# Kernel tuning notes

Measured on AMD Instinct MI355X. Metric: run time of the kernel, lower is better.

Reference implementation:

```python
import jax, jax.numpy as jnp
import numpy as np

D_LOW = 32
LAGS = [1, 2, 4, 8]
# Upper-triangular pair indices (offset=1), matching torch.triu_indices(d_low, d_low, 1)
IDX_I, IDX_J = np.triu_indices(D_LOW, k=1)
IDX_I = jnp.asarray(IDX_I)
IDX_J = jnp.asarray(IDX_J)
EPS = 1e-6


def setup_inputs() -> dict:
    key = jax.random.key(0)
    ks = jax.random.split(key, 7)
    b, n, d_model = 4, 4096, 1024
    d_plucker = D_LOW * (D_LOW - 1) // 2  # 496
    s = lambda fan_in: 1.0 / np.sqrt(fan_in)
    return {
        "x": jax.random.normal(ks[0], (b, n, d_model), dtype=jnp.float32),
        "W_red": jax.random.normal(ks[1], (d_model, D_LOW), dtype=jnp.float32) * s(d_model),
        "b_red": jax.random.normal(ks[2], (D_LOW,), dtype=jnp.float32) * s(d_model),
        "W_exp": jax.random.normal(ks[3], (d_plucker, d_model), dtype=jnp.float32) * s(d_plucker),
        "b_exp": jax.random.normal(ks[4], (d_model,), dtype=jnp.float32) * s(d_plucker),
        "W_gate": jax.random.normal(ks[5], (2 * d_model, d_model), dtype=jnp.float32) * s(2 * d_model),
        "b_gate": jax.random.normal(ks[6], (d_model,), dtype=jnp.float32) * s(2 * d_model),
    }


def reference(x, W_red, b_red, W_exp, b_exp, W_gate, b_gate):
    b, n, _ = x.shape
    d_plucker = D_LOW * (D_LOW - 1) // 2
    z = x @ W_red + b_red  # [b, n, d_low]
    plucker_total = jnp.zeros((b, n, d_plucker), dtype=x.dtype)
    counts = jnp.zeros((b, n, 1), dtype=x.dtype)
    for lag in LAGS:
        if lag <= 0 or lag >= n:
            continue
        z_curr = z[:, lag:, :]   # [b, n-lag, d_low]
        z_past = z[:, :-lag, :]  # [b, n-lag, d_low]
        # Antisymmetric Plucker coordinates over upper-triangular index pairs
        p = (z_curr[:, :, IDX_I] * z_past[:, :, IDX_J]
             - z_curr[:, :, IDX_J] * z_past[:, :, IDX_I])  # [b, n-lag, d_plucker]
        norm = jnp.linalg.norm(p, axis=-1, keepdims=True)
        p = p / jnp.maximum(norm, EPS)
        plucker_total = plucker_total.at[:, lag:, :].add(p)
        counts = counts.at[:, lag:, :].add(1.0)
    counts = jnp.maximum(counts, 1.0)
    plucker_avg = plucker_total / counts
    g_avg = plucker_avg @ W_exp + b_exp  # [b, n, d_model]
    concat = jnp.concatenate([x, g_avg], axis=-1)  # [b, n, 2*d_model]
    gate = jax.nn.sigmoid(concat @ W_gate + b_gate)
    return gate * x + (1.0 - gate) * g_avg
```

## Files before the change

### kernel.cpp

```cpp
#include <hip/hip_runtime.h>
#include <hip/hip_bf16.h>
#include <math.h>

#define B_DIM   4
#define N_DIM   4096
#define D_MODEL 1024
#define D_LOW   32
#define NPAIR   496
#define NROWS   (B_DIM * N_DIM)
#define KPAD3   512
#define LDA2    1536

typedef __bf16 bf16;
typedef __bf16 bf16x8 __attribute__((ext_vector_type(8)));
typedef __bf16 bf16x4 __attribute__((ext_vector_type(4)));
typedef float  f32x4  __attribute__((ext_vector_type(4)));

#define GLOAD_LDS16(g, l) __builtin_amdgcn_global_load_lds( \
    (__attribute__((address_space(1))) void*)(g),           \
    (__attribute__((address_space(3))) void*)(l), 16, 0, 0)

__global__ __launch_bounds__(256) void wred_t(const float* __restrict__ Wr,
                                              bf16* __restrict__ WrT) {
    __shared__ float tile[32][33];
    const int t  = threadIdx.x;
    const int kb = blockIdx.x * 32;
    {
        int k = t >> 3, c4 = (t & 7) * 4;
        float4 v = *reinterpret_cast<const float4*>(&Wr[(size_t)(kb + k) * 32 + c4]);
        tile[k][c4 + 0] = v.x; tile[k][c4 + 1] = v.y;
        tile[k][c4 + 2] = v.z; tile[k][c4 + 3] = v.w;
    }
    __syncthreads();
    {
        int c = t >> 3, kq = (t & 7) * 4;
        bf16x4 o = { (bf16)tile[kq + 0][c], (bf16)tile[kq + 1][c],
                     (bf16)tile[kq + 2][c], (bf16)tile[kq + 3][c] };
        *reinterpret_cast<bf16x4*>(&WrT[(size_t)c * 1024 + kb + kq]) = o;
    }
}

__global__ __launch_bounds__(256) void k1_mfma(const float* __restrict__ x,
                                               const bf16* __restrict__ WrT,
                                               bf16* __restrict__ a2,
                                               float* __restrict__ zpart) {
    const int t    = threadIdx.x;
    const int wv   = t >> 6, lane = t & 63;
    const int l15  = lane & 15, lhi = lane >> 4;
    const int kc   = blockIdx.x;
    const int mt   = blockIdx.y;
    const int row  = mt * 64 + wv * 16 + l15;
    const int kb   = kc * 512;

    f32x4 accz[2] = { (f32x4){0.f,0.f,0.f,0.f}, (f32x4){0.f,0.f,0.f,0.f} };

#pragma unroll
    for (int ks = 0; ks < 16; ++ks) {
        const int k0 = kb + ks * 32 + lhi * 8;
        const float4 u0 = *reinterpret_cast<const float4*>(&x[(size_t)row * 1024 + k0]);
        const float4 u1 = *reinterpret_cast<const float4*>(&x[(size_t)row * 1024 + k0 + 4]);
        bf16x8 af = { (bf16)u0.x, (bf16)u0.y, (bf16)u0.z, (bf16)u0.w,
                      (bf16)u1.x, (bf16)u1.y, (bf16)u1.z, (bf16)u1.w };
        *reinterpret_cast<bf16x8*>(&a2[(size_t)row * LDA2 + k0]) = af;
        const bf16x8 b0 = *reinterpret_cast<const bf16x8*>(
            &WrT[(size_t)l15 * 1024 + kb + ks * 32 + lhi * 8]);
        const bf16x8 b1 = *reinterpret_cast<const bf16x8*>(
            &WrT[(size_t)(16 + l15) * 1024 + kb + ks * 32 + lhi * 8]);
        accz[0] = __builtin_amdgcn_mfma_f32_16x16x32_bf16(af, b0, accz[0], 0, 0, 0);
        accz[1] = __builtin_amdgcn_mfma_f32_16x16x32_bf16(af, b1, accz[1], 0, 0, 0);
    }
#pragma unroll
    for (int cg = 0; cg < 2; ++cg)
#pragma unroll
        for (int r = 0; r < 4; ++r) {
            const int rout = mt * 64 + wv * 16 + lhi * 4 + r;
            zpart[((size_t)kc * NROWS + rout) * 32 + cg * 16 + l15] = accz[cg][r];
        }
}

__global__ __launch_bounds__(256) void k2_plucker(const float* __restrict__ zpart,
                                                  const float* __restrict__ br,
                                                  bf16* __restrict__ a2) {
    const int wv   = threadIdx.x >> 6;
    const int lane = threadIdx.x & 63;
    const int row  = blockIdx.x * 4 + wv;
    const int t    = row & (N_DIM - 1);
    const int c    = lane & 31;
    const float bias = br[c];

    float zc = bias;
#pragma unroll
    for (int p = 0; p < 2; ++p)
        zc += zpart[((size_t)p * NROWS + row) * 32 + c];

    float zp[4];
    float red[9];
    red[0] = zc * zc;
#pragma unroll
    for (int li = 0; li < 4; ++li) {
        const int lag = 1 << li;
        float v = 0.f;
        if (t >= lag) {
            v = bias;
#pragma unroll
            for (int p = 0; p < 2; ++p)
                v += zpart[((size_t)p * NROWS + (row - lag)) * 32 + c];
        }
        zp[li] = v;
        red[1 + li] = zc * zp[li];
        red[5 + li] = zp[li] * zp[li];
    }
#pragma unroll
    for (int m = 1; m < 32; m <<= 1) {
#pragma unroll
        for (int i = 0; i < 9; ++i) red[i] += __shfl_xor(red[i], m);
    }
    float cnt = 0.f;
#pragma unroll
    for (int li = 0; li < 4; ++li) cnt += (t >= (1 << li)) ? 1.f : 0.f;
    const float inv = 1.f / fmaxf(cnt, 1.f);

    float w = 0.f;
#pragma unroll
    for (int li = 0; li < 4; ++li) {
        float n2 = fmaxf(red[0] * red[5 + li] - red[1 + li] * red[1 + li], 0.f);
        float nr = sqrtf(n2);
        float s  = (t >= (1 << li)) ? inv / fmaxf(nr, 1e-6f) : 0.f;
        w += s * zp[li];
    }

#pragma unroll
    for (int u = 0; u < 8; ++u) {
        const int k = u * 64 + lane;
        float v = 0.f;
        if (k < NPAIR) {
            int kk = k, i = 0;
            while (kk >= 31 - i) { kk -= 31 - i; ++i; }
            const int j = i + 1 + kk;
            float zci = __shfl(zc, i), zcj = __shfl(zc, j);
            float wi  = __shfl(w, i),  wj  = __shfl(w, j);
            v = zci * wj - zcj * wi;
        }
        a2[(size_t)row * LDA2 + 1024 + k] = (bf16)v;
    }
}

__global__ __launch_bounds__(256) void transpose_cvt(const float* __restrict__ src,
                                                     bf16* __restrict__ dst,
                                                     int Ksrc, int Kpad) {
    __shared__ float tile[32][36];
    const int t  = threadIdx.x;
    const int kb = blockIdx.x * 32;
    const int nb = blockIdx.y * 32;
    int li = t * 4;
    int kl = li >> 5, nl = li & 31;
    float4 v = {0.f, 0.f, 0.f, 0.f};
    if (kb + kl < Ksrc)
        v = *reinterpret_cast<const float4*>(&src[(size_t)(kb + kl) * 1024 + nb + nl]);
    tile[kl][nl + 0] = v.x; tile[kl][nl + 1] = v.y;
    tile[kl][nl + 2] = v.z; tile[kl][nl + 3] = v.w;
    __syncthreads();
    int nl2 = li >> 5, kl2 = li & 31;
    bf16x4 o = { (bf16)tile[kl2 + 0][nl2], (bf16)tile[kl2 + 1][nl2],
                 (bf16)tile[kl2 + 2][nl2], (bf16)tile[kl2 + 3][nl2] };
    *reinterpret_cast<bf16x4*>(&dst[(size_t)(nb + nl2) * Kpad + kb + kl2]) = o;
}

__global__ __launch_bounds__(256) void we_cvt_be(const float* __restrict__ We,
                                                 const float* __restrict__ be,
                                                 bf16* __restrict__ WeB) {
    size_t o = ((size_t)blockIdx.x * 256 + threadIdx.x) * 4;
    int row = (int)(o >> 10), col = (int)(o & 1023);
    float4 v = {0.f, 0.f, 0.f, 0.f};
    if (row < NPAIR)      v = *reinterpret_cast<const float4*>(&We[(size_t)row * 1024 + col]);
    else if (row == NPAIR) v = *reinterpret_cast<const float4*>(&be[col]);
    bf16x4 b = { (bf16)v.x, (bf16)v.y, (bf16)v.z, (bf16)v.w };
    *reinterpret_cast<bf16x4*>(&WeB[o]) = b;
}

__global__ __launch_bounds__(256) void wcomb_mfma(const bf16* __restrict__ A,
                                                  const bf16* __restrict__ Bt,
                                                  bf16* __restrict__ BcT) {
    __shared__ bf16 As[128 * 32];
    __shared__ bf16 Bs[128 * 32];
    const int t    = threadIdx.x;
    const int mb   = blockIdx.y * 128;
    const int nbq  = blockIdx.x * 128;
    const int w    = t >> 6, lane = t & 63;
    const int wr   = w >> 1, wc = w & 1;
    const int l15  = lane & 15, lhi = lane >> 4;

    f32x4 acc[4][4];
#pragma unroll
    for (int mt = 0; mt < 4; ++mt)
#pragma unroll
        for (int nt = 0; nt < 4; ++nt) acc[mt][nt] = (f32x4){0.f, 0.f, 0.f, 0.f};

    const int li0 = t, li1 = t + 256;
    const int r0 = li0 >> 2, c0 = (li0 & 3) * 8;
    const int r1 = li1 >> 2, c1 = (li1 & 3) * 8;

    for (int kb = 0; kb < 1024; kb += 32) {
        GLOAD_LDS16(A  + (size_t)(mb + r0) * 1024 + kb + c0, As + li0 * 8);
        GLOAD_LDS16(A  + (size_t)(mb + r1) * 1024 + kb + c1, As + li1 * 8);
        GLOAD_LDS16(Bt + (size_t)(nbq + r0) * 1024 + kb + c0, Bs + li0 * 8);
        GLOAD_LDS16(Bt + (size_t)(nbq + r1) * 1024 + kb + c1, Bs + li1 * 8);
        __syncthreads();
        bf16x8 a[4], b[4];
#pragma unroll
        for (int mt = 0; mt < 4; ++mt)
            a[mt] = *reinterpret_cast<const bf16x8*>(
                As + (wr * 64 + mt * 16 + l15) * 32 + lhi * 8);
#pragma unroll
        for (int nt = 0; nt < 4; ++nt)
            b[nt] = *reinterpret_cast<const bf16x8*>(
                Bs + (wc * 64 + nt * 16 + l15) * 32 + lhi * 8);
#pragma unroll
        for (int mt = 0; mt < 4; ++mt)
#pragma unroll
            for (int nt = 0; nt < 4; ++nt)
                acc[mt][nt] = __builtin_amdgcn_mfma_f32_16x16x32_bf16(
                    a[mt], b[nt], acc[mt][nt], 0, 0, 0);
        __syncthreads();
    }
#pragma unroll
    for (int mt = 0; mt < 4; ++mt)
#pragma unroll
        for (int nt = 0; nt < 4; ++nt) {
            const int col = nbq + wc * 64 + nt * 16 + l15;
#pragma unroll
            for (int r = 0; r < 4; ++r) {
                const int row = mb + wr * 64 + mt * 16 + lhi * 4 + r;
                BcT[(size_t)row * 1536 + 1024 + col] = (bf16)acc[mt][nt][r];
            }
        }
}

__global__ __launch_bounds__(256) void bgc_extract(const float* __restrict__ bg,
                                                   const bf16* __restrict__ BcT,
                                                   float* __restrict__ bgc) {
    int n = blockIdx.x * 256 + threadIdx.x;
    bgc[n] = bg[n] + (float)BcT[(size_t)n * 1536 + 1024 + NPAIR];
}

template <int KDIM, int LDAp, int LDBp, bool GATE>
__global__ __launch_bounds__(512, 2) void gemmzr(const bf16* __restrict__ A,
                                                 const bf16* __restrict__ Bt,
                                                 const float* __restrict__ bias,
                                                 const bf16* __restrict__ gsrc,
                                                 bf16* __restrict__ gdst,
                                                 float* __restrict__ out) {
    extern __shared__ char lds[];
    const int t    = threadIdx.x;
    const int w    = t >> 6, lane = t & 63;
    const int wr   = w >> 2, wc = w & 3;
    const int l15  = lane & 15, lhi = lane >> 4;

    const int fid = blockIdx.x;
    const int xcd = fid & 7, loc = fid >> 3;
    const int mb  = (xcd * 8 + (loc >> 2)) * 256;
    const int nb  = (loc & 3) * 256;

    const int srow = t >> 3;
    const int scol = ((t & 7) ^ (srow & 7)) * 8;
    const size_t aOff = (size_t)(mb + srow) * LDAp + scol;
    const size_t bOff = (size_t)(nb + srow) * LDBp + scol;
    char* const ldsA = lds;
    char* const ldsB = lds + 65536;

#define STAGE_A(d, h, kb) do { \
    GLOAD_LDS16(A + aOff + (size_t)((h) * 128) * LDAp + (kb),      ldsA + (d) * 32768 + (h) * 16384 + t * 16); \
    GLOAD_LDS16(A + aOff + (size_t)((h) * 128 + 64) * LDAp + (kb), ldsA + (d) * 32768 + (h) * 16384 + 8192 + t * 16); } while (0)
#define STAGE_B(d, h, kb) do { \
    GLOAD_LDS16(Bt + bOff + (size_t)((h) * 128) * LDBp + (kb),      ldsB + (d) * 32768 + (h) * 16384 + t * 16); \
    GLOAD_LDS16(Bt + bOff + (size_t)((h) * 128 + 64) * LDBp + (kb), ldsB + (d) * 32768 + (h) * 16384 + 8192 + t * 16); } while (0)

    const int swx = (l15 & 7) << 4;
#define LDAF(d, mq_) do { const char* Ab_ = ldsA + (d) * 32768 + wr * 16384; \
    _Pragma("unroll") for (int mf = 0; mf < 4; ++mf) \
    _Pragma("unroll") for (int ks = 0; ks < 2; ++ks) { \
        int lin = ((mq_) * 64 + mf * 16 + l15) * 128 + ks * 64 + lhi * 16; \
        afr[mf][ks] = *reinterpret_cast<const bf16x8*>(Ab_ + (lin ^ swx)); } } while (0)
#define LDBF(dst, d, nq_) do { const char* Bb_ = ldsB + (d) * 32768 + (wc >> 1) * 16384; \
    _Pragma("unroll") for (int nf = 0; nf < 2; ++nf) \
    _Pragma("unroll") for (int ks = 0; ks < 2; ++ks) { \
        int lin = ((wc & 1) * 64 + (nq_) * 32 + nf * 16 + l15) * 128 + ks * 64 + lhi * 16; \
        dst[nf][ks] = *reinterpret_cast<const bf16x8*>(Bb_ + (lin ^ swx)); } } while (0)
#define MMA(bset, mq_, nq_) do { __builtin_amdgcn_s_setprio(1); \
    _Pragma("unroll") for (int mf = 0; mf < 4; ++mf) \
    _Pragma("unroll") for (int nf = 0; nf < 2; ++nf) \
    _Pragma("unroll") for (int ks = 0; ks < 2; ++ks) \
        acc[(mq_) * 4 + mf][(nq_) * 2 + nf] = __builtin_amdgcn_mfma_f32_16x16x32_bf16( \
            afr[mf][ks], bset[nf][ks], acc[(mq_) * 4 + mf][(nq_) * 2 + nf], 0, 0, 0); \
    __builtin_amdgcn_s_setprio(0); } while (0)
#define BAR() asm volatile("s_barrier" ::: "memory")

    f32x4 acc[8][4];
#pragma unroll
    for (int i = 0; i < 8; ++i)
#pragma unroll
        for (int j = 0; j < 4; ++j) acc[i][j] = (f32x4){0.f, 0.f, 0.f, 0.f};
    bf16x8 afr[4][2], bfr0[2][2], bfrB[2][2];

    STAGE_A(0, 0, 0);  STAGE_A(0, 1, 0);  STAGE_B(0, 0, 0);  STAGE_B(0, 1, 0);
    STAGE_A(1, 0, 64); STAGE_A(1, 1, 64); STAGE_B(1, 0, 64); STAGE_B(1, 1, 64);

    const int NT    = KDIM / 64;
    const int ITERS = NT / 2;
    for (int it = 0; it < ITERS; ++it) {
        const int kA = (it * 2 + 2) * 64;
        const int kB = (it * 2 + 3) * 64;
        const bool p2 = (it * 2 + 2) < NT;
        const bool p3 = (it * 2 + 3) < NT;

        asm volatile("s_waitcnt vmcnt(8)" ::: "memory");
        BAR();
        LDAF(0, 0); LDBF(bfr0, 0, 0);
        MMA(bfr0, 0, 0);
        BAR();
        LDBF(bfrB, 0, 1);
        MMA(bfrB, 0, 1);
        BAR();
        if (p2) { STAGE_B(0, 0, kA); STAGE_B(0, 1, kA); }
        LDAF(0, 1);
        MMA(bfrB, 1, 1);
        BAR();
        if (p2) { STAGE_A(0, 0, kA); STAGE_A(0, 1, kA); }
        MMA(bfr0, 1, 0);

        if (p2) asm volatile("s_waitcnt vmcnt(8)" ::: "memory");
        else    asm volatile("s_waitcnt vmcnt(0)" ::: "memory");
        BAR();
        LDAF(1, 0); LDBF(bfr0, 1, 0);
        MMA(bfr0, 0, 0);
        BAR();
        LDBF(bfrB, 1, 1);
        MMA(bfrB, 0, 1);
        BAR();
        if (p3) { STAGE_B(1, 0, kB); STAGE_B(1, 1, kB); }
        LDAF(1, 1);
        MMA(bfrB, 1, 1);
        BAR();
        if (p3) { STAGE_A(1, 0, kB); STAGE_A(1, 1, kB); }
        MMA(bfr0, 1, 0);
    }
#undef STAGE_A
#undef STAGE_B
#undef LDAF
#undef LDBF
#undef MMA
#undef BAR

#pragma unroll
    for (int mi = 0; mi < 8; ++mi) {
#pragma unroll
        for (int nf = 0; nf < 4; ++nf) {
            const int col = nb + wc * 64 + nf * 16 + l15;
            const float bv = bias[col];
#pragma unroll
            for (int r = 0; r < 4; ++r) {
                const int row = mb + wr * 128 + mi * 16 + lhi * 4 + r;
                float v = acc[mi][nf][r] + bv;
                if constexpr (GATE) {
                    float gate = 1.f / (1.f + expf(-v));
                    float xv = (float)A[(size_t)row * LDAp + col];
                    float gv = (float)gsrc[(size_t)row * D_MODEL + col];
                    out[(size_t)row * D_MODEL + col] = gate * xv + (1.f - gate) * gv;
                } else {
                    gdst[(size_t)row * D_MODEL + col] = (bf16)v;
                }
            }
        }
    }
}

extern "C" void kernel_launch(void* const* d_in, const int* in_sizes, int n_in,
                              void* d_out, int out_size, void* d_ws, size_t ws_size,
                              hipStream_t stream) {
    const float* x  = (const float*)d_in[0];
    const float* Wr = (const float*)d_in[1];
    const float* br = (const float*)d_in[2];
    const float* We = (const float*)d_in[3];
    const float* be = (const float*)d_in[4];
    const float* Wg = (const float*)d_in[5];
    const float* bg = (const float*)d_in[6];
    float* out = (float*)d_out;

    char* ws = (char*)d_ws;
    bf16*  gbuf  = (bf16*)(ws);
    float* zpart = (float*)(ws);
    bf16*  A2    = (bf16*)(ws + (32u << 20));
    bf16*  WeT   = (bf16*)(ws + (80u << 20));
    bf16*  BcT   = (bf16*)(ws + (81u << 20));
    bf16*  WgbT  = (bf16*)(ws + (84u << 20));
    bf16*  WeB   = (bf16*)(ws + (86u << 20));
    float* bgc   = (float*)(ws + (87u << 20));
    bf16*  WrT   = (bf16*)(ws + (88u << 20));

    (void)hipFuncSetAttribute(reinterpret_cast<const void*>(&gemmzr<KPAD3, LDA2, KPAD3, false>),
                              hipFuncAttributeMaxDynamicSharedMemorySize, 131072);
    (void)hipFuncSetAttribute(reinterpret_cast<const void*>(&gemmzr<1536, LDA2, 1536, true>),
                              hipFuncAttributeMaxDynamicSharedMemorySize, 131072);

    wred_t<<<32, 256, 0, stream>>>(Wr, WrT);
    k1_mfma<<<dim3(2, 256), 256, 0, stream>>>(x, WrT, A2, zpart);
    k2_plucker<<<NROWS / 4, 256, 0, stream>>>(zpart, br, A2);

    transpose_cvt<<<dim3(KPAD3 / 32, 1024 / 32), 256, 0, stream>>>(We, WeT, NPAIR, KPAD3);
    transpose_cvt<<<dim3(1024 / 32, 1024 / 32), 256, 0, stream>>>(Wg, BcT, 1024, 1536);
    transpose_cvt<<<dim3(1024 / 32, 1024 / 32), 256, 0, stream>>>(Wg + (size_t)1024 * 1024, WgbT, 1024, 1024);
    we_cvt_be<<<512, 256, 0, stream>>>(We, be, WeB);
    wcomb_mfma<<<dim3(4, 8), 256, 0, stream>>>(WgbT, WeB, BcT);
    bgc_extract<<<4, 256, 0, stream>>>(bg, BcT, bgc);

    gemmzr<KPAD3, LDA2, KPAD3, false><<<256, 512, 131072, stream>>>(
        A2 + 1024, WeT, be, nullptr, gbuf, nullptr);
    gemmzr<1536, LDA2, 1536, true><<<256, 512, 131072, stream>>>(
        A2, BcT, bgc, gbuf, nullptr, out);
}
```

Before: 164.6 us.

## Merge weight-prep kernels and fold gate bias extraction into GEMM epilogue

Cuts the launch count of the weight-preparation stage. The Wr transpose and the We/be conversion become one kernel, and the three transpose_cvt calls become one 3D-grid kernel. The weight-combine GEMM is rewritten as a smaller per-wave MFMA kernel with no LDS and many more blocks, and the separate bias-extract kernel is dropped by reading the folded bias column inside the gated GEMM epilogue. The aim is lower launch and serialization overhead plus better parallelism for the small GEMM, at the cost of uncached direct global loads in the combine kernel.

```diff
diff --git a/kernel.cpp b/kernel.cpp
--- a/kernel.cpp
+++ b/kernel.cpp
@@ -20,23 +20,37 @@
     (__attribute__((address_space(1))) void*)(g),           \
     (__attribute__((address_space(3))) void*)(l), 16, 0, 0)
 
-__global__ __launch_bounds__(256) void wred_t(const float* __restrict__ Wr,
-                                              bf16* __restrict__ WrT) {
+__global__ __launch_bounds__(256) void prep_misc(const float* __restrict__ Wr,
+                                                 bf16* __restrict__ WrT,
+                                                 const float* __restrict__ We,
+                                                 const float* __restrict__ be,
+                                                 bf16* __restrict__ WeB) {
     __shared__ float tile[32][33];
+    const int bx = blockIdx.x;
     const int t  = threadIdx.x;
-    const int kb = blockIdx.x * 32;
-    {
-        int k = t >> 3, c4 = (t & 7) * 4;
-        float4 v = *reinterpret_cast<const float4*>(&Wr[(size_t)(kb + k) * 32 + c4]);
-        tile[k][c4 + 0] = v.x; tile[k][c4 + 1] = v.y;
-        tile[k][c4 + 2] = v.z; tile[k][c4 + 3] = v.w;
-    }
-    __syncthreads();
-    {
-        int c = t >> 3, kq = (t & 7) * 4;
-        bf16x4 o = { (bf16)tile[kq + 0][c], (bf16)tile[kq + 1][c],
-                     (bf16)tile[kq + 2][c], (bf16)tile[kq + 3][c] };
-        *reinterpret_cast<bf16x4*>(&WrT[(size_t)c * 1024 + kb + kq]) = o;
+    if (bx < 32) {
+        const int kb = bx * 32;
+        {
+            int k = t >> 3, c4 = (t & 7) * 4;
+            float4 v = *reinterpret_cast<const float4*>(&Wr[(size_t)(kb + k) * 32 + c4]);
+            tile[k][c4 + 0] = v.x; tile[k][c4 + 1] = v.y;
+            tile[k][c4 + 2] = v.z; tile[k][c4 + 3] = v.w;
+        }
+        __syncthreads();
+        {
+            int c = t >> 3, kq = (t & 7) * 4;
+            bf16x4 o = { (bf16)tile[kq + 0][c], (bf16)tile[kq + 1][c],
+                         (bf16)tile[kq + 2][c], (bf16)tile[kq + 3][c] };
+            *reinterpret_cast<bf16x4*>(&WrT[(size_t)c * 1024 + kb + kq]) = o;
+        }
+    } else {
+        size_t o = ((size_t)(bx - 32) * 256 + t) * 4;
+        int row = (int)(o >> 10), col = (int)(o & 1023);
+        float4 v = {0.f, 0.f, 0.f, 0.f};
+        if (row < NPAIR)       v = *reinterpret_cast<const float4*>(&We[(size_t)row * 1024 + col]);
+        else if (row == NPAIR) v = *reinterpret_cast<const float4*>(&be[col]);
+        bf16x4 b = { (bf16)v.x, (bf16)v.y, (bf16)v.z, (bf16)v.w };
+        *reinterpret_cast<bf16x4*>(&WeB[o]) = b;
     }
 }
 
@@ -145,13 +159,21 @@
     }
 }
 
-__global__ __launch_bounds__(256) void transpose_cvt(const float* __restrict__ src,
-                                                     bf16* __restrict__ dst,
-                                                     int Ksrc, int Kpad) {
+__global__ __launch_bounds__(256) void transpose2(const float* __restrict__ Wg,
+                                                  const float* __restrict__ We,
+                                                  bf16* __restrict__ BcT,
+                                                  bf16* __restrict__ WgbT,
+                                                  bf16* __restrict__ WeT) {
     __shared__ float tile[32][36];
+    const int z = blockIdx.z;
+    const float* src = (z == 0) ? Wg : (z == 1) ? (Wg + (size_t)1024 * 1024) : We;
+    bf16* dst  = (z == 0) ? BcT : (z == 1) ? WgbT : WeT;
+    const int Kpad = (z == 0) ? 1536 : (z == 1) ? 1024 : 512;
+    const int Ksrc = (z == 2) ? NPAIR : 1024;
+    const int kb = blockIdx.x * 32;
+    if (kb >= Kpad) return;
+    const int nb = blockIdx.y * 32;
     const int t  = threadIdx.x;
-    const int kb = blockIdx.x * 32;
-    const int nb = blockIdx.y * 32;
     int li = t * 4;
     int kl = li >> 5, nl = li & 31;
     float4 v = {0.f, 0.f, 0.f, 0.f};
@@ -166,81 +188,28 @@
     *reinterpret_cast<bf16x4*>(&dst[(size_t)(nb + nl2) * Kpad + kb + kl2]) = o;
 }
 
-__global__ __launch_bounds__(256) void we_cvt_be(const float* __restrict__ We,
-                                                 const float* __restrict__ be,
-                                                 bf16* __restrict__ WeB) {
-    size_t o = ((size_t)blockIdx.x * 256 + threadIdx.x) * 4;
-    int row = (int)(o >> 10), col = (int)(o & 1023);
-    float4 v = {0.f, 0.f, 0.f, 0.f};
-    if (row < NPAIR)      v = *reinterpret_cast<const float4*>(&We[(size_t)row * 1024 + col]);
-    else if (row == NPAIR) v = *reinterpret_cast<const float4*>(&be[col]);
-    bf16x4 b = { (bf16)v.x, (bf16)v.y, (bf16)v.z, (bf16)v.w };
-    *reinterpret_cast<bf16x4*>(&WeB[o]) = b;
-}
-
-__global__ __launch_bounds__(256) void wcomb_mfma(const bf16* __restrict__ A,
-                                                  const bf16* __restrict__ Bt,
+__global__ __launch_bounds__(256) void wcomb_wave(const bf16* __restrict__ WgbT,
+                                                  const bf16* __restrict__ WeB,
                                                   bf16* __restrict__ BcT) {
-    __shared__ bf16 As[128 * 32];
-    __shared__ bf16 Bs[128 * 32];
     const int t    = threadIdx.x;
-    const int mb   = blockIdx.y * 128;
-    const int nbq  = blockIdx.x * 128;
-    const int w    = t >> 6, lane = t & 63;
-    const int wr   = w >> 1, wc = w & 1;
+    const int wv   = t >> 6, lane = t & 63;
     const int l15  = lane & 15, lhi = lane >> 4;
-
-    f32x4 acc[4][4];
-#pragma unroll
-    for (int mt = 0; mt < 4; ++mt)
-#pragma unroll
-        for (int nt = 0; nt < 4; ++nt) acc[mt][nt] = (f32x4){0.f, 0.f, 0.f, 0.f};
-
-    const int li0 = t, li1 = t + 256;
-    const int r0 = li0 >> 2, c0 = (li0 & 3) * 8;
-    const int r1 = li1 >> 2, c1 = (li1 & 3) * 8;
-
+    const int kk0  = blockIdx.x * 16;
+    const int n0   = blockIdx.y * 64 + wv * 16;
+    f32x4 acc = (f32x4){0.f, 0.f, 0.f, 0.f};
+#pragma unroll 8
     for (int kb = 0; kb < 1024; kb += 32) {
-        GLOAD_LDS16(A  + (size_t)(mb + r0) * 1024 + kb + c0, As + li0 * 8);
-        GLOAD_LDS16(A  + (size_t)(mb + r1) * 1024 + kb + c1, As + li1 * 8);
-        GLOAD_LDS16(Bt + (size_t)(nbq + r0) * 1024 + kb + c0, Bs + li0 * 8);
-        GLOAD_LDS16(Bt + (size_t)(nbq + r1) * 1024 + kb + c1, Bs + li1 * 8);
-        __syncthreads();
-        bf16x8 a[4], b[4];
-#pragma unroll
-        for (int mt = 0; mt < 4; ++mt)
-            a[mt] = *reinterpret_cast<const bf16x8*>(
-                As + (wr * 64 + mt * 16 + l15) * 32 + lhi * 8);
-#pragma unroll
-        for (int nt = 0; nt < 4; ++nt)
-            b[nt] = *reinterpret_cast<const bf16x8*>(
-                Bs + (wc * 64 + nt * 16 + l15) * 32 + lhi * 8);
-#pragma unroll
-        for (int mt = 0; mt < 4; ++mt)
-#pragma unroll
-            for (int nt = 0; nt < 4; ++nt)
-                acc[mt][nt] = __builtin_amdgcn_mfma_f32_16x16x32_bf16(
-                    a[mt], b[nt], acc[mt][nt], 0, 0, 0);
-        __syncthreads();
-    }
-#pragma unroll
-    for (int mt = 0; mt < 4; ++mt)
-#pragma unroll
-        for (int nt = 0; nt < 4; ++nt) {
-            const int col = nbq + wc * 64 + nt * 16 + l15;
-#pragma unroll
-            for (int r = 0; r < 4; ++r) {
-                const int row = mb + wr * 64 + mt * 16 + lhi * 4 + r;
-                BcT[(size_t)row * 1536 + 1024 + col] = (bf16)acc[mt][nt][r];
-            }
-        }
-}
-
-__global__ __launch_bounds__(256) void bgc_extract(const float* __restrict__ bg,
-                                                   const bf16* __restrict__ BcT,
-                                                   float* __restrict__ bgc) {
-    int n = blockIdx.x * 256 + threadIdx.x;
-    bgc[n] = bg[n] + (float)BcT[(size_t)n * 1536 + 1024 + NPAIR];
+        const bf16x8 af = *reinterpret_cast<const bf16x8*>(
+            &WgbT[(size_t)(n0 + l15) * 1024 + kb + lhi * 8]);
+        const bf16x8 bf = *reinterpret_cast<const bf16x8*>(
+            &WeB[(size_t)(kk0 + l15) * 1024 + kb + lhi * 8]);
+        acc = __builtin_amdgcn_mfma_f32_16x16x32_bf16(af, bf, acc, 0, 0, 0);
+    }
+#pragma unroll
+    for (int r = 0; r < 4; ++r) {
+        const int n = n0 + lhi * 4 + r;
+        BcT[(size_t)n * 1536 + 1024 + kk0 + l15] = (bf16)acc[r];
+    }
 }
 
 template <int KDIM, int LDAp, int LDBp, bool GATE>
@@ -356,7 +325,9 @@
 #pragma unroll
         for (int nf = 0; nf < 4; ++nf) {
             const int col = nb + wc * 64 + nf * 16 + l15;
-            const float bv = bias[col];
+            float bv = bias[col];
+            if constexpr (GATE)
+                bv += (float)Bt[(size_t)col * LDBp + 1024 + NPAIR];
 #pragma unroll
             for (int r = 0; r < 4; ++r) {
                 const int row = mb + wr * 128 + mi * 16 + lhi * 4 + r;
@@ -394,7 +365,6 @@
     bf16*  BcT   = (bf16*)(ws + (81u << 20));
     bf16*  WgbT  = (bf16*)(ws + (84u << 20));
     bf16*  WeB   = (bf16*)(ws + (86u << 20));
-    float* bgc   = (float*)(ws + (87u << 20));
     bf16*  WrT   = (bf16*)(ws + (88u << 20));
 
     (void)hipFuncSetAttribute(reinterpret_cast<const void*>(&gemmzr<KPAD3, LDA2, KPAD3, false>),
@@ -402,19 +372,14 @@
     (void)hipFuncSetAttribute(reinterpret_cast<const void*>(&gemmzr<1536, LDA2, 1536, true>),
                               hipFuncAttributeMaxDynamicSharedMemorySize, 131072);
 
-    wred_t<<<32, 256, 0, stream>>>(Wr, WrT);
+    prep_misc<<<544, 256, 0, stream>>>(Wr, WrT, We, be, WeB);
+    transpose2<<<dim3(32, 32, 3), 256, 0, stream>>>(Wg, We, BcT, WgbT, WeT);
+    wcomb_wave<<<dim3(32, 16), 256, 0, stream>>>(WgbT, WeB, BcT);
     k1_mfma<<<dim3(2, 256), 256, 0, stream>>>(x, WrT, A2, zpart);
     k2_plucker<<<NROWS / 4, 256, 0, stream>>>(zpart, br, A2);
-
-    transpose_cvt<<<dim3(KPAD3 / 32, 1024 / 32), 256, 0, stream>>>(We, WeT, NPAIR, KPAD3);
-    transpose_cvt<<<dim3(1024 / 32, 1024 / 32), 256, 0, stream>>>(Wg, BcT, 1024, 1536);
-    transpose_cvt<<<dim3(1024 / 32, 1024 / 32), 256, 0, stream>>>(Wg + (size_t)1024 * 1024, WgbT, 1024, 1024);
-    we_cvt_be<<<512, 256, 0, stream>>>(We, be, WeB);
-    wcomb_mfma<<<dim3(4, 8), 256, 0, stream>>>(WgbT, WeB, BcT);
-    bgc_extract<<<4, 256, 0, stream>>>(bg, BcT, bgc);
 
     gemmzr<KPAD3, LDA2, KPAD3, false><<<256, 512, 131072, stream>>>(
         A2 + 1024, WeT, be, nullptr, gbuf, nullptr);
     gemmzr<1536, LDA2, 1536, true><<<256, 512, 131072, stream>>>(
-        A2, BcT, bgc, gbuf, nullptr, out);
-}
+        A2, BcT, bg, gbuf, nullptr, out);
+}
```

New measurement: 163.2 us. Within noise of the previous version (-0.8%).
